# Kernel optimization log

Hardware: AMD Instinct MI355X
Metric: run time of the kernel (lower is better)

Reference implementation:

```python
import jax, jax.numpy as jnp
import numpy as np

HIDDEN = 4096
N_HEADS = 32
N_KV = 32
HEAD_DIM = HIDDEN // N_HEADS  # 128
T = 2048
THETA = 10000.0
EPS = 1e-5


def setup_inputs() -> dict:
    key = jax.random.key(0)
    ks = jax.random.split(key, 7)
    s = 0.02
    return {
        "positions": jnp.arange(T, dtype=jnp.int64),
        "hidden_states": jax.random.normal(ks[0], (T, HIDDEN), jnp.float32),
        "w_qkv": jax.random.normal(ks[1], ((N_HEADS + 2 * N_KV) * HEAD_DIM, HIDDEN), jnp.float32) * s,
        "w_o": jax.random.normal(ks[2], (HIDDEN, N_HEADS * HEAD_DIM), jnp.float32) * s,
        "q_norm_w": jnp.ones((N_HEADS, HEAD_DIM), jnp.float32) + jax.random.normal(ks[3], (N_HEADS, HEAD_DIM), jnp.float32) * s,
        "q_norm_b": jax.random.normal(ks[4], (N_HEADS, HEAD_DIM), jnp.float32) * s,
        "k_norm_w": jnp.ones((N_KV, HEAD_DIM), jnp.float32) + jax.random.normal(ks[5], (N_KV, HEAD_DIM), jnp.float32) * s,
        "k_norm_b": jax.random.normal(ks[6], (N_KV, HEAD_DIM), jnp.float32) * s,
    }


def _layer_norm_affine(x, w, b):
    # x: [T, H, d]; normalize over last dim, no affine inside, then per-head affine
    mu = jnp.mean(x, axis=-1, keepdims=True)
    var = jnp.var(x, axis=-1, keepdims=True)
    xn = (x - mu) * jax.lax.rsqrt(var + EPS)
    return xn * w + b


def _rope_neox(x, positions):
    # x: [T, H, d], NEOX style: rotate halves over full head_dim
    half = HEAD_DIM // 2
    inv_freq = 1.0 / (THETA ** (jnp.arange(0, half, dtype=jnp.float32) * 2.0 / HEAD_DIM))
    ang = positions.astype(jnp.float32)[:, None] * inv_freq  # [T, half]
    cos = jnp.cos(ang)[:, None, :]
    sin = jnp.sin(ang)[:, None, :]
    x1, x2 = x[..., :half], x[..., half:]
    return jnp.concatenate([x1 * cos - x2 * sin, x2 * cos + x1 * sin], axis=-1)


def reference(positions, hidden_states, w_qkv, w_o, q_norm_w, q_norm_b, k_norm_w, k_norm_b):
    qkv = hidden_states @ w_qkv.T  # [T, (H+2Hkv)*d]
    q_size = N_HEADS * HEAD_DIM
    kv_size = N_KV * HEAD_DIM
    q = qkv[:, :q_size].reshape(T, N_HEADS, HEAD_DIM)
    k = qkv[:, q_size:q_size + kv_size].reshape(T, N_KV, HEAD_DIM)
    v = qkv[:, q_size + kv_size:].reshape(T, N_KV, HEAD_DIM)

    q = _layer_norm_affine(q, q_norm_w, q_norm_b)
    k = _layer_norm_affine(k, k_norm_w, k_norm_b)
    q = _rope_neox(q, positions)
    k = _rope_neox(k, positions)

    scale = HEAD_DIM ** -0.5
    scores = jnp.einsum('thd,shd->hts', q, k) * scale  # [H, T, T]
    causal = jnp.tril(jnp.ones((T, T), dtype=bool))
    scores = jnp.where(causal[None], scores, jnp.finfo(scores.dtype).min)
    p = jax.nn.softmax(scores, axis=-1)
    attn = jnp.einsum('hts,shd->thd', p, v).reshape(T, N_HEADS * HEAD_DIM)
    return attn @ w_o.T
```

## Files before the change

### kernel.cpp

```cpp
#include <hip/hip_runtime.h>
#include <cstdint>

#define T_SEQ 2048
#define HID   4096
#define NH    32
#define HD    128
#define QKVW  12288

typedef float  f32x4  __attribute__((ext_vector_type(4)));
typedef __bf16 bf16x8 __attribute__((ext_vector_type(8)));

#define QSCALE (0.08838834764831845f * 1.4426950408889634f)

__device__ __forceinline__ unsigned short f2bf(float f) {
  unsigned int u = __builtin_bit_cast(unsigned int, f);
  u += 0x7fffu + ((u >> 16) & 1u);
  return (unsigned short)(u >> 16);
}
__device__ __forceinline__ float bf2f(unsigned short u) {
  return __builtin_bit_cast(float, (unsigned int)u << 16);
}

__device__ __forceinline__ void gload_lds16(const void* gptr, void* lptr) {
  __builtin_amdgcn_global_load_lds(
      (const __attribute__((address_space(1))) unsigned int*)(unsigned long long)(uintptr_t)gptr,
      (__attribute__((address_space(3))) unsigned int*)(unsigned int)(uintptr_t)lptr,
      16, 0, 0);
}

#define SB __builtin_amdgcn_sched_barrier(0)

__global__ __launch_bounds__(256) void cast_bf16(const float* __restrict__ in,
                                                 unsigned short* __restrict__ out,
                                                 int n4) {
  int i = blockIdx.x * 256 + threadIdx.x;
  int stride = gridDim.x * 256;
  for (; i < n4; i += stride) {
    float4 v = ((const float4*)in)[i];
    ushort4 o;
    o.x = f2bf(v.x); o.y = f2bf(v.y); o.z = f2bf(v.z); o.w = f2bf(v.w);
    ((ushort4*)out)[i] = o;
  }
}

__global__ __launch_bounds__(512, 2) void gemm_bt(const unsigned short* __restrict__ Ag,
                                                  const unsigned short* __restrict__ Bg,
                                                  float* __restrict__ C,
                                                  int M, int N, int K, int MT) {
  __shared__ unsigned short As_[2][128 * 64];
  __shared__ unsigned short Bs_[2][256 * 64];
  const int tid  = threadIdx.x;
  const int lane = tid & 63;
  const int w    = tid >> 6;
  const int wm   = w >> 2;
  const int wn   = w & 3;
  const int l15  = lane & 15;
  const int lg   = lane >> 4;

  const int nwg = gridDim.x;
  const int cpx = nwg >> 3;
  const int swz = (blockIdx.x & 7) * cpx + (blockIdx.x >> 3);
  const int bm  = (swz % MT) * 128;
  const int bn  = (swz / MT) * 256;
  const int nk  = K >> 6;

#define STAGE_A(buf, kt_) do {                                                   \
    const unsigned short* _s = Ag + (size_t)bm * K + (size_t)(kt_) * 64;         \
    _Pragma("unroll")                                                            \
    for (int _u = 0; _u < 2; ++_u) {                                             \
      const int _cid = _u * 512 + tid;                                           \
      const int _r = _cid >> 3, _ch = _cid & 7;                                  \
      gload_lds16(_s + (size_t)_r * K + ((_ch ^ (_r & 7)) * 8),                  \
                  &As_[buf][(_u * 512 + w * 64) * 8]);                           \
    } } while (0)

#define STAGE_B(buf, kt_) do {                                                   \
    const unsigned short* _s = Bg + (size_t)bn * K + (size_t)(kt_) * 64;         \
    _Pragma("unroll")                                                            \
    for (int _u = 0; _u < 4; ++_u) {                                             \
      const int _cid = _u * 512 + tid;                                           \
      const int _r = _cid >> 3, _ch = _cid & 7;                                  \
      gload_lds16(_s + (size_t)_r * K + ((_ch ^ (_r & 7)) * 8),                  \
                  &Bs_[buf][(_u * 512 + w * 64) * 8]);                           \
    } } while (0)

  f32x4 acc[4][4] = {};

  STAGE_A(0, 0);
  STAGE_B(0, 0);
  if (nk > 1) {
    STAGE_B(1, 1);
    asm volatile("s_waitcnt vmcnt(4)" ::: "memory");
  } else {
    asm volatile("s_waitcnt vmcnt(0)" ::: "memory");
  }
  __builtin_amdgcn_s_barrier();

  for (int t = 0; t < nk; ++t) {
    const int cur = t & 1;
    bf16x8 bfr[4][2];
#pragma unroll
    for (int n = 0; n < 4; ++n)
#pragma unroll
      for (int kk = 0; kk < 2; ++kk) {
        const int r = wn * 64 + n * 16 + l15;
        bfr[n][kk] = *(const bf16x8*)&Bs_[cur][r * 64 + (((kk * 4 + lg) ^ (r & 7)) * 8)];
      }
    bf16x8 a0[2][2];
#pragma unroll
    for (int mi = 0; mi < 2; ++mi)
#pragma unroll
      for (int kk = 0; kk < 2; ++kk) {
        const int r = wm * 64 + mi * 16 + l15;
        a0[mi][kk] = *(const bf16x8*)&As_[cur][r * 64 + (((kk * 4 + lg) ^ (r & 7)) * 8)];
      }
    if (t + 1 < nk) STAGE_A(cur ^ 1, t + 1);
    __builtin_amdgcn_s_barrier();
    __builtin_amdgcn_s_setprio(1);
#pragma unroll
    for (int mi = 0; mi < 2; ++mi)
#pragma unroll
      for (int n = 0; n < 4; ++n)
#pragma unroll
        for (int kk = 0; kk < 2; ++kk)
          acc[mi][n] = __builtin_amdgcn_mfma_f32_16x16x32_bf16(a0[mi][kk], bfr[n][kk], acc[mi][n], 0, 0, 0);
    __builtin_amdgcn_s_setprio(0);
    __builtin_amdgcn_s_barrier();

    bf16x8 a1[2][2];
#pragma unroll
    for (int mi = 0; mi < 2; ++mi)
#pragma unroll
      for (int kk = 0; kk < 2; ++kk) {
        const int r = wm * 64 + (2 + mi) * 16 + l15;
        a1[mi][kk] = *(const bf16x8*)&As_[cur][r * 64 + (((kk * 4 + lg) ^ (r & 7)) * 8)];
      }
    if (t + 2 < nk) STAGE_B(cur, t + 2);
    __builtin_amdgcn_s_barrier();
    __builtin_amdgcn_s_setprio(1);
#pragma unroll
    for (int mi = 0; mi < 2; ++mi)
#pragma unroll
      for (int n = 0; n < 4; ++n)
#pragma unroll
        for (int kk = 0; kk < 2; ++kk)
          acc[2 + mi][n] = __builtin_amdgcn_mfma_f32_16x16x32_bf16(a1[mi][kk], bfr[n][kk], acc[2 + mi][n], 0, 0, 0);
    __builtin_amdgcn_s_setprio(0);
    if (t + 1 < nk) {
      if (t + 2 < nk) asm volatile("s_waitcnt vmcnt(4)" ::: "memory");
      else            asm volatile("s_waitcnt vmcnt(0)" ::: "memory");
      __builtin_amdgcn_sched_barrier(0);
    }
    __builtin_amdgcn_s_barrier();
  }
#undef STAGE_A
#undef STAGE_B

#pragma unroll
  for (int m = 0; m < 4; ++m)
#pragma unroll
    for (int i = 0; i < 4; ++i) {
      const int row = bm + wm * 64 + m * 16 + lg * 4 + i;
#pragma unroll
      for (int n = 0; n < 4; ++n)
        C[(size_t)row * N + bn + wn * 64 + n * 16 + l15] = acc[m][n][i];
    }
}

__global__ __launch_bounds__(512, 2) void gemm_bt8(const unsigned short* __restrict__ Ag,
                                                   const unsigned short* __restrict__ Bg,
                                                   unsigned short* __restrict__ C,
                                                   int M, int N, int K, int MT) {
  __shared__ unsigned short As_[2][256 * 64];
  __shared__ unsigned short Bs_[2][192 * 64];
  const int tid  = threadIdx.x;
  const int lane = tid & 63;
  const int w    = tid >> 6;
  const int wm   = w & 3;
  const int wn   = w >> 2;
  const int l15  = lane & 15;
  const int lg   = lane >> 4;
  const int sw   = l15 & 7;

  const int cpx = gridDim.x >> 3;
  const int swz = (blockIdx.x & 7) * cpx + (blockIdx.x >> 3);
  const int bm  = (swz % MT) * 256;
  const int bn  = (swz / MT) * 192;
  const int nk  = K >> 6;

  const unsigned short* Abase = Ag + (size_t)bm * K;
  const unsigned short* Bbase = Bg + (size_t)bn * K;

#define SG(ldsbase, gbase, kt_, u_) do {                                        \
    const int _cid = (u_) * 512 + tid;                                          \
    const int _r = _cid >> 3, _ch = _cid & 7;                                   \
    gload_lds16((gbase) + (size_t)_r * K + (size_t)(kt_) * 64 +                 \
                    ((_ch ^ (_r & 7)) * 8),                                     \
                (void*)((char*)(ldsbase) + _cid * 16));                         \
  } while (0)
#define STAGE(abuf, bbuf, kt_) do {                                             \
    SG(abuf, Abase, kt_, 0); SG(abuf, Abase, kt_, 1);                           \
    SG(abuf, Abase, kt_, 2); SG(abuf, Abase, kt_, 3);                           \
    SG(bbuf, Bbase, kt_, 0); SG(bbuf, Bbase, kt_, 1);                           \
    SG(bbuf, Bbase, kt_, 2);                                                    \
  } while (0)

#define RD(base, r, kk)                                                          \
  (*(const bf16x8*)((const char*)(base) + (r) * 128 + ((((kk) * 4 + lg) ^ sw) * 16)))

#define MFMA24(afr, bfr) do {                                                    \
    _Pragma("unroll")                                                            \
    for (int _m = 0; _m < 4; ++_m)                                               \
      _Pragma("unroll")                                                          \
      for (int _n = 0; _n < 6; ++_n)                                             \
        acc[_m][_n] = __builtin_amdgcn_mfma_f32_16x16x32_bf16(                   \
            afr[_m], bfr[_n], acc[_m][_n], 0, 0, 0);                             \
  } while (0)

  f32x4 acc[4][6] = {};

  STAGE(As_[0], Bs_[0], 0);
  if (nk > 1) {
    STAGE(As_[1], Bs_[1], 1);
    asm volatile("s_waitcnt vmcnt(7)" ::: "memory");
  } else {
    asm volatile("s_waitcnt vmcnt(0)" ::: "memory");
  }
  SB;
  __builtin_amdgcn_s_barrier();

  for (int t = 0; t < nk; ++t) {
    const int cur = t & 1;
    const unsigned short* As = As_[cur];
    const unsigned short* Bs = Bs_[cur];
    bf16x8 a0[4], a1[4], b0[6], b1[6];

#pragma unroll
    for (int m = 0; m < 4; ++m) a0[m] = RD(As, wm * 64 + m * 16 + l15, 0);
#pragma unroll
    for (int n = 0; n < 6; ++n) b0[n] = RD(Bs, wn * 96 + n * 16 + l15, 0);
    SB;
#pragma unroll
    for (int m = 0; m < 4; ++m) a1[m] = RD(As, wm * 64 + m * 16 + l15, 1);
#pragma unroll
    for (int n = 0; n < 6; ++n) b1[n] = RD(Bs, wn * 96 + n * 16 + l15, 1);
    SB;
    asm volatile("s_waitcnt lgkmcnt(10)" ::: "memory");
    SB;
    __builtin_amdgcn_s_setprio(1);
    MFMA24(a0, b0);
    __builtin_amdgcn_s_setprio(0);
    SB;
    asm volatile("s_waitcnt lgkmcnt(0)" ::: "memory");
    SB;
    __builtin_amdgcn_s_barrier();
    if (t + 2 < nk) STAGE(As_[cur], Bs_[cur], t + 2);
    SB;
    __builtin_amdgcn_s_setprio(1);
    MFMA24(a1, b1);
    __builtin_amdgcn_s_setprio(0);
    if (t + 1 < nk) {
      if (t + 2 < nk) asm volatile("s_waitcnt vmcnt(7)" ::: "memory");
      else            asm volatile("s_waitcnt vmcnt(0)" ::: "memory");
      SB;
      __builtin_amdgcn_s_barrier();
    }
  }
#undef SG
#undef STAGE
#undef RD
#undef MFMA24

#pragma unroll
  for (int m = 0; m < 4; ++m)
#pragma unroll
    for (int i = 0; i < 4; ++i) {
      const int row = bm + wm * 64 + m * 16 + lg * 4 + i;
#pragma unroll
      for (int n = 0; n < 6; ++n)
        C[(size_t)row * N + bn + wn * 96 + n * 16 + l15] = f2bf(acc[m][n][i]);
    }
}

__global__ __launch_bounds__(256) void norm_rope(const unsigned short* __restrict__ qkv,
                                                 const float* __restrict__ qw,
                                                 const float* __restrict__ qb,
                                                 const float* __restrict__ kw,
                                                 const float* __restrict__ kb,
                                                 unsigned short* __restrict__ q,
                                                 unsigned short* __restrict__ k) {
  const int t    = blockIdx.x;
  const int tid  = threadIdx.x;
  const int lane = tid & 63;
  const int w    = tid >> 6;
  const float invf = exp2f(-(float)lane * (13.287712379549449f / 64.0f));
  const float ang  = (float)t * invf;
  const float c = cosf(ang), s = sinf(ang);
  const unsigned short* row = qkv + (size_t)t * QKVW;

#pragma unroll 1
  for (int sel = 0; sel < 2; ++sel) {
    const unsigned short* src = row + sel * HID;
    const float* wgt = sel ? kw : qw;
    const float* bia = sel ? kb : qb;
    unsigned short* dst = sel ? k : q;
    const float oscale = sel ? 1.0f : QSCALE;
    for (int h = w; h < NH; h += 4) {
      const unsigned short* x = src + h * HD;
      float x1 = bf2f(x[lane]), x2 = bf2f(x[lane + 64]);
      float sum = x1 + x2, ss = x1 * x1 + x2 * x2;
#pragma unroll
      for (int m = 1; m < 64; m <<= 1) {
        sum += __shfl_xor(sum, m, 64);
        ss  += __shfl_xor(ss, m, 64);
      }
      const float mu  = sum * (1.0f / 128.0f);
      const float var = ss * (1.0f / 128.0f) - mu * mu;
      const float r   = rsqrtf(var + 1e-5f);
      const float n1  = (x1 - mu) * r * wgt[h * HD + lane]      + bia[h * HD + lane];
      const float n2  = (x2 - mu) * r * wgt[h * HD + lane + 64] + bia[h * HD + lane + 64];
      const float o1  = (n1 * c - n2 * s) * oscale;
      const float o2  = (n2 * c + n1 * s) * oscale;
      dst[(size_t)t * HID + h * HD + lane]      = f2bf(o1);
      dst[(size_t)t * HID + h * HD + lane + 64] = f2bf(o2);
    }
  }
}

__global__ __launch_bounds__(256) void transpose_v(const unsigned short* __restrict__ v,
                                                   unsigned short* __restrict__ vt) {
  __shared__ unsigned short tile[64][65];
  const int h  = blockIdx.z;
  const int tt = blockIdx.x * 64;
  const int dd = blockIdx.y * 64;
  const int tid = threadIdx.x;
#pragma unroll
  for (int p = 0; p < 4; ++p) {
    int idx = p * 256 + tid;
    int r = idx >> 4, c4 = idx & 15;
    ushort4 val = *(const ushort4*)&v[(size_t)(tt + r) * QKVW + h * HD + dd + c4 * 4];
    tile[r][c4 * 4 + 0] = val.x;
    tile[r][c4 * 4 + 1] = val.y;
    tile[r][c4 * 4 + 2] = val.z;
    tile[r][c4 * 4 + 3] = val.w;
  }
  __syncthreads();
#pragma unroll
  for (int p = 0; p < 4; ++p) {
    int idx = p * 256 + tid;
    int r = idx >> 4, c4 = idx & 15;
    ushort4 o;
    o.x = tile[c4 * 4 + 0][r];
    o.y = tile[c4 * 4 + 1][r];
    o.z = tile[c4 * 4 + 2][r];
    o.w = tile[c4 * 4 + 3][r];
    *(ushort4*)&vt[((size_t)h * HD + dd + r) * T_SEQ + tt + c4 * 4] = o;
  }
}

__global__ __launch_bounds__(256) void attn_fwd(const unsigned short* __restrict__ Q,
                                                const unsigned short* __restrict__ K,
                                                const unsigned short* __restrict__ VT,
                                                unsigned short* __restrict__ O) {
  __shared__ unsigned short Ks[2][64 * 128];
  __shared__ unsigned short Vs[2][128 * 64];
  __shared__ unsigned short Ps[4][16 * 64];
  const int h    = blockIdx.y;
  const int pair = blockIdx.x;
  const int tid  = threadIdx.x;
  const int lane = tid & 63;
  const int w    = tid >> 6;
  const int l15  = lane & 15;
  const int lg   = lane >> 4;
  const int sw   = l15 & 7;

#pragma unroll 1
  for (int half = 0; half < 2; ++half) {
    const int qt   = half ? (31 - pair) : pair;
    const int qrow = qt * 64 + w * 16;

    bf16x8 qf[4];
#pragma unroll
    for (int kk = 0; kk < 4; ++kk)
      qf[kk] = *(const bf16x8*)&Q[(size_t)(qrow + l15) * HID + h * HD + kk * 32 + lg * 8];

    f32x4 o[8] = {};
    float mrow[4], lrow[4];
#pragma unroll
    for (int i = 0; i < 4; ++i) { mrow[i] = -1e30f; lrow[i] = 0.0f; }

    const int nkt = qt + 1;

    {
#pragma unroll
      for (int p = 0; p < 4; ++p) {
        const int c  = p * 256 + tid;
        const int kr = c >> 4, kc = c & 15;
        gload_lds16(&K[(size_t)kr * HID + h * HD + ((kc ^ (kr & 7)) * 8)],
                    &Ks[0][(p * 256 + w * 64) * 8]);
        const int vr = c >> 3, vc = c & 7;
        gload_lds16(&VT[((size_t)h * HD + vr) * T_SEQ + ((vc ^ (vr & 7)) * 8)],
                    &Vs[0][(p * 256 + w * 64) * 8]);
      }
    }
    __syncthreads();

#pragma unroll 1
    for (int kt = 0; kt < nkt; ++kt) {
      const int cur = kt & 1;
      if (kt + 1 < nkt) {
        const int k0 = (kt + 1) * 64;
#pragma unroll
        for (int p = 0; p < 4; ++p) {
          const int c  = p * 256 + tid;
          const int kr = c >> 4, kc = c & 15;
          gload_lds16(&K[(size_t)(k0 + kr) * HID + h * HD + ((kc ^ (kr & 7)) * 8)],
                      &Ks[cur ^ 1][(p * 256 + w * 64) * 8]);
          const int vr = c >> 3, vc = c & 7;
          gload_lds16(&VT[((size_t)h * HD + vr) * T_SEQ + k0 + ((vc ^ (vr & 7)) * 8)],
                      &Vs[cur ^ 1][(p * 256 + w * 64) * 8]);
        }
      }
      const unsigned short* ksb = Ks[cur];
      const unsigned short* vsb = Vs[cur];

      f32x4 sfr[4] = {};
#pragma unroll
      for (int n = 0; n < 4; ++n)
#pragma unroll
        for (int kk = 0; kk < 4; ++kk) {
          bf16x8 kf = *(const bf16x8*)&ksb[(n * 16 + l15) * 128 + ((kk * 4 + lg) ^ sw) * 8];
          sfr[n] = __builtin_amdgcn_mfma_f32_16x16x32_bf16(qf[kk], kf, sfr[n], 0, 0, 0);
        }

      if (kt == qt) {
#pragma unroll
        for (int n = 0; n < 4; ++n)
#pragma unroll
          for (int i = 0; i < 4; ++i)
            if (n * 16 + l15 > w * 16 + lg * 4 + i) sfr[n][i] = -1e30f;
      }

      float escale[4];
#pragma unroll
      for (int i = 0; i < 4; ++i) {
        float mx = fmaxf(fmaxf(sfr[0][i], sfr[1][i]), fmaxf(sfr[2][i], sfr[3][i]));
        mx = fmaxf(mx, __shfl_xor(mx, 1, 64));
        mx = fmaxf(mx, __shfl_xor(mx, 2, 64));
        mx = fmaxf(mx, __shfl_xor(mx, 4, 64));
        mx = fmaxf(mx, __shfl_xor(mx, 8, 64));
        const float mnew = fmaxf(mrow[i], mx);
        escale[i] = exp2f(mrow[i] - mnew);
        mrow[i] = mnew;
        const int prow = lg * 4 + i;
        float rs = 0.0f;
#pragma unroll
        for (int n = 0; n < 4; ++n) {
          const float p = exp2f(sfr[n][i] - mnew);
          rs += p;
          Ps[w][prow * 64 + (((2 * n + (l15 >> 3)) ^ (prow & 7)) * 8) + sw] = f2bf(p);
        }
        rs += __shfl_xor(rs, 1, 64);
        rs += __shfl_xor(rs, 2, 64);
        rs += __shfl_xor(rs, 4, 64);
        rs += __shfl_xor(rs, 8, 64);
        lrow[i] = lrow[i] * escale[i] + rs;
      }
#pragma unroll
      for (int f = 0; f < 8; ++f)
#pragma unroll
        for (int i = 0; i < 4; ++i) o[f][i] *= escale[i];

      asm volatile("s_waitcnt lgkmcnt(0)" ::: "memory");
      __builtin_amdgcn_sched_barrier(0);

      bf16x8 pf[2];
#pragma unroll
      for (int kk = 0; kk < 2; ++kk)
        pf[kk] = *(const bf16x8*)&Ps[w][l15 * 64 + ((kk * 4 + lg) ^ sw) * 8];
#pragma unroll
      for (int f = 0; f < 8; ++f)
#pragma unroll
        for (int kk = 0; kk < 2; ++kk) {
          bf16x8 vf = *(const bf16x8*)&vsb[(f * 16 + l15) * 64 + ((kk * 4 + lg) ^ sw) * 8];
          o[f] = __builtin_amdgcn_mfma_f32_16x16x32_bf16(pf[kk], vf, o[f], 0, 0, 0);
        }

      __syncthreads();
    }

#pragma unroll
    for (int i = 0; i < 4; ++i) {
      const float inv = 1.0f / lrow[i];
      const int trow = qrow + lg * 4 + i;
#pragma unroll
      for (int f = 0; f < 8; ++f)
        O[(size_t)trow * HID + h * HD + f * 16 + l15] = f2bf(o[f][i] * inv);
    }
  }
}

extern "C" void kernel_launch(void* const* d_in, const int* in_sizes, int n_in,
                              void* d_out, int out_size, void* d_ws, size_t ws_size,
                              hipStream_t stream) {
  const float* hidden = (const float*)d_in[1];
  const float* w_qkv  = (const float*)d_in[2];
  const float* w_o    = (const float*)d_in[3];
  const float* qw     = (const float*)d_in[4];
  const float* qb     = (const float*)d_in[5];
  const float* kw     = (const float*)d_in[6];
  const float* kb     = (const float*)d_in[7];

  char* ws = (char*)d_ws;
  unsigned short* wqkv_bf = (unsigned short*)(ws + 0);
  unsigned short* attn_bf = (unsigned short*)(ws + 0);
  unsigned short* wo_bf   = (unsigned short*)(ws + 16777216);
  unsigned short* hid_bf  = (unsigned short*)(ws + 100663296);
  unsigned short* vt_bf   = (unsigned short*)(ws + 100663296);
  unsigned short* qkv_bf  = (unsigned short*)(ws + 117440512);
  unsigned short* q_bf    = (unsigned short*)(ws + 167772160);
  unsigned short* k_bf    = (unsigned short*)(ws + 184549376);

  cast_bf16<<<2048, 256, 0, stream>>>(hidden, hid_bf, (T_SEQ * HID) / 4);
  cast_bf16<<<2048, 256, 0, stream>>>(w_qkv, wqkv_bf, (QKVW * HID) / 4);
  gemm_bt8<<<512, 512, 0, stream>>>(hid_bf, wqkv_bf, qkv_bf, T_SEQ, QKVW, HID, 8);
  cast_bf16<<<2048, 256, 0, stream>>>(w_o, wo_bf, (HID * HID) / 4);
  norm_rope<<<T_SEQ, 256, 0, stream>>>(qkv_bf, qw, qb, kw, kb, q_bf, k_bf);
  transpose_v<<<dim3(T_SEQ / 64, HD / 64, NH), 256, 0, stream>>>(qkv_bf + 2 * HID, vt_bf);
  attn_fwd<<<dim3(16, NH), 256, 0, stream>>>(q_bf, k_bf, vt_bf, attn_bf);
  gemm_bt<<<256, 512, 0, stream>>>(attn_bf, wo_bf, (float*)d_out, T_SEQ, HID, HID, 16);
}
```

Measured before the change: 463.8 us.

## Process two 16-row query fragments per warp in attention to reuse K/V tiles

Each warp now computes 32 query rows (two MFMA fragments) against each K/V tile, so a block covers 128 queries and the grid halves. This doubles MFMA work per LDS K/V fragment load and halves the global K/V traffic per query. In exchange it raises register pressure and halves the number of blocks, reducing occupancy and latency hiding.

After: 489.5 us. 5.6% more time.

```diff
diff --git a/kernel.cpp b/kernel.cpp
--- a/kernel.cpp
+++ b/kernel.cpp
@@ -364,9 +364,9 @@
                                                 unsigned short* __restrict__ O) {
   __shared__ unsigned short Ks[2][64 * 128];
   __shared__ unsigned short Vs[2][128 * 64];
-  __shared__ unsigned short Ps[4][16 * 64];
+  __shared__ unsigned short Ps[4][2][16 * 64];
   const int h    = blockIdx.y;
-  const int pair = blockIdx.x;
+  const int pr   = blockIdx.x;
   const int tid  = threadIdx.x;
   const int lane = tid & 63;
   const int w    = tid >> 6;
@@ -376,20 +376,24 @@
 
 #pragma unroll 1
   for (int half = 0; half < 2; ++half) {
-    const int qt   = half ? (31 - pair) : pair;
-    const int qrow = qt * 64 + w * 16;
-
-    bf16x8 qf[4];
-#pragma unroll
-    for (int kk = 0; kk < 4; ++kk)
-      qf[kk] = *(const bf16x8*)&Q[(size_t)(qrow + l15) * HID + h * HD + kk * 32 + lg * 8];
-
-    f32x4 o[8] = {};
-    float mrow[4], lrow[4];
-#pragma unroll
-    for (int i = 0; i < 4; ++i) { mrow[i] = -1e30f; lrow[i] = 0.0f; }
-
-    const int nkt = qt + 1;
+    const int jt    = half ? (15 - pr) : pr;
+    const int qbase = jt * 128 + w * 32;
+
+    bf16x8 qf[2][4];
+#pragma unroll
+    for (int f = 0; f < 2; ++f)
+#pragma unroll
+      for (int kk = 0; kk < 4; ++kk)
+        qf[f][kk] = *(const bf16x8*)&Q[(size_t)(qbase + f * 16 + l15) * HID + h * HD + kk * 32 + lg * 8];
+
+    f32x4 o[2][8] = {};
+    float mrow[2][4], lrow[2][4];
+#pragma unroll
+    for (int f = 0; f < 2; ++f)
+#pragma unroll
+      for (int i = 0; i < 4; ++i) { mrow[f][i] = -1e30f; lrow[f][i] = 0.0f; }
+
+    const int nkt = 2 * (jt + 1);
 
     {
 #pragma unroll
@@ -424,79 +428,91 @@
       const unsigned short* ksb = Ks[cur];
       const unsigned short* vsb = Vs[cur];
 
-      f32x4 sfr[4] = {};
+      f32x4 sfr[2][4] = {};
 #pragma unroll
       for (int n = 0; n < 4; ++n)
 #pragma unroll
         for (int kk = 0; kk < 4; ++kk) {
           bf16x8 kf = *(const bf16x8*)&ksb[(n * 16 + l15) * 128 + ((kk * 4 + lg) ^ sw) * 8];
-          sfr[n] = __builtin_amdgcn_mfma_f32_16x16x32_bf16(qf[kk], kf, sfr[n], 0, 0, 0);
+          sfr[0][n] = __builtin_amdgcn_mfma_f32_16x16x32_bf16(qf[0][kk], kf, sfr[0][n], 0, 0, 0);
+          sfr[1][n] = __builtin_amdgcn_mfma_f32_16x16x32_bf16(qf[1][kk], kf, sfr[1][n], 0, 0, 0);
         }
 
-      if (kt == qt) {
-#pragma unroll
-        for (int n = 0; n < 4; ++n)
-#pragma unroll
-          for (int i = 0; i < 4; ++i)
-            if (n * 16 + l15 > w * 16 + lg * 4 + i) sfr[n][i] = -1e30f;
-      }
-
-      float escale[4];
-#pragma unroll
-      for (int i = 0; i < 4; ++i) {
-        float mx = fmaxf(fmaxf(sfr[0][i], sfr[1][i]), fmaxf(sfr[2][i], sfr[3][i]));
-        mx = fmaxf(mx, __shfl_xor(mx, 1, 64));
-        mx = fmaxf(mx, __shfl_xor(mx, 2, 64));
-        mx = fmaxf(mx, __shfl_xor(mx, 4, 64));
-        mx = fmaxf(mx, __shfl_xor(mx, 8, 64));
-        const float mnew = fmaxf(mrow[i], mx);
-        escale[i] = exp2f(mrow[i] - mnew);
-        mrow[i] = mnew;
-        const int prow = lg * 4 + i;
-        float rs = 0.0f;
-#pragma unroll
-        for (int n = 0; n < 4; ++n) {
-          const float p = exp2f(sfr[n][i] - mnew);
-          rs += p;
-          Ps[w][prow * 64 + (((2 * n + (l15 >> 3)) ^ (prow & 7)) * 8) + sw] = f2bf(p);
+      if (kt >= 2 * jt) {
+#pragma unroll
+        for (int f = 0; f < 2; ++f)
+#pragma unroll
+          for (int n = 0; n < 4; ++n)
+#pragma unroll
+            for (int i = 0; i < 4; ++i)
+              if (kt * 64 + n * 16 + l15 > qbase + f * 16 + lg * 4 + i) sfr[f][n][i] = -1e30f;
+      }
+
+#pragma unroll
+      for (int f = 0; f < 2; ++f) {
+        float escale[4];
+#pragma unroll
+        for (int i = 0; i < 4; ++i) {
+          float mx = fmaxf(fmaxf(sfr[f][0][i], sfr[f][1][i]), fmaxf(sfr[f][2][i], sfr[f][3][i]));
+          mx = fmaxf(mx, __shfl_xor(mx, 1, 64));
+          mx = fmaxf(mx, __shfl_xor(mx, 2, 64));
+          mx = fmaxf(mx, __shfl_xor(mx, 4, 64));
+          mx = fmaxf(mx, __shfl_xor(mx, 8, 64));
+          const float mnew = fmaxf(mrow[f][i], mx);
+          escale[i] = exp2f(mrow[f][i] - mnew);
+          mrow[f][i] = mnew;
+          const int prow = lg * 4 + i;
+          float rs = 0.0f;
+#pragma unroll
+          for (int n = 0; n < 4; ++n) {
+            const float p = exp2f(sfr[f][n][i] - mnew);
+            rs += p;
+            Ps[w][f][prow * 64 + (((2 * n + (l15 >> 3)) ^ (prow & 7)) * 8) + sw] = f2bf(p);
+          }
+          rs += __shfl_xor(rs, 1, 64);
+          rs += __shfl_xor(rs, 2, 64);
+          rs += __shfl_xor(rs, 4, 64);
+          rs += __shfl_xor(rs, 8, 64);
+          lrow[f][i] = lrow[f][i] * escale[i] + rs;
         }
-        rs += __shfl_xor(rs, 1, 64);
-        rs += __shfl_xor(rs, 2, 64);
-        rs += __shfl_xor(rs, 4, 64);
-        rs += __shfl_xor(rs, 8, 64);
-        lrow[i] = lrow[i] * escale[i] + rs;
-      }
-#pragma unroll
-      for (int f = 0; f < 8; ++f)
-#pragma unroll
-        for (int i = 0; i < 4; ++i) o[f][i] *= escale[i];
+#pragma unroll
+        for (int fd = 0; fd < 8; ++fd)
+#pragma unroll
+          for (int i = 0; i < 4; ++i) o[f][fd][i] *= escale[i];
+      }
 
       asm volatile("s_waitcnt lgkmcnt(0)" ::: "memory");
       __builtin_amdgcn_sched_barrier(0);
 
-      bf16x8 pf[2];
-#pragma unroll
-      for (int kk = 0; kk < 2; ++kk)
-        pf[kk] = *(const bf16x8*)&Ps[w][l15 * 64 + ((kk * 4 + lg) ^ sw) * 8];
-#pragma unroll
-      for (int f = 0; f < 8; ++f)
+      bf16x8 pf[2][2];
+#pragma unroll
+      for (int f = 0; f < 2; ++f)
+#pragma unroll
+        for (int kk = 0; kk < 2; ++kk)
+          pf[f][kk] = *(const bf16x8*)&Ps[w][f][l15 * 64 + ((kk * 4 + lg) ^ sw) * 8];
+
+#pragma unroll
+      for (int fd = 0; fd < 8; ++fd)
 #pragma unroll
         for (int kk = 0; kk < 2; ++kk) {
-          bf16x8 vf = *(const bf16x8*)&vsb[(f * 16 + l15) * 64 + ((kk * 4 + lg) ^ sw) * 8];
-          o[f] = __builtin_amdgcn_mfma_f32_16x16x32_bf16(pf[kk], vf, o[f], 0, 0, 0);
+          bf16x8 vf = *(const bf16x8*)&vsb[(fd * 16 + l15) * 64 + ((kk * 4 + lg) ^ sw) * 8];
+          o[0][fd] = __builtin_amdgcn_mfma_f32_16x16x32_bf16(pf[0][kk], vf, o[0][fd], 0, 0, 0);
+          o[1][fd] = __builtin_amdgcn_mfma_f32_16x16x32_bf16(pf[1][kk], vf, o[1][fd], 0, 0, 0);
         }
 
       __syncthreads();
     }
 
 #pragma unroll
-    for (int i = 0; i < 4; ++i) {
-      const float inv = 1.0f / lrow[i];
-      const int trow = qrow + lg * 4 + i;
-#pragma unroll
-      for (int f = 0; f < 8; ++f)
-        O[(size_t)trow * HID + h * HD + f * 16 + l15] = f2bf(o[f][i] * inv);
-    }
+    for (int f = 0; f < 2; ++f)
+#pragma unroll
+      for (int i = 0; i < 4; ++i) {
+        const float inv = 1.0f / lrow[f][i];
+        const int trow = qbase + f * 16 + lg * 4 + i;
+#pragma unroll
+        for (int fd = 0; fd < 8; ++fd)
+          O[(size_t)trow * HID + h * HD + fd * 16 + l15] = f2bf(o[f][fd][i] * inv);
+      }
   }
 }
 
@@ -527,6 +543,6 @@
   cast_bf16<<<2048, 256, 0, stream>>>(w_o, wo_bf, (HID * HID) / 4);
   norm_rope<<<T_SEQ, 256, 0, stream>>>(qkv_bf, qw, qb, kw, kb, q_bf, k_bf);
   transpose_v<<<dim3(T_SEQ / 64, HD / 64, NH), 256, 0, stream>>>(qkv_bf + 2 * HID, vt_bf);
-  attn_fwd<<<dim3(16, NH), 256, 0, stream>>>(q_bf, k_bf, vt_bf, attn_bf);
+  attn_fwd<<<dim3(8, NH), 256, 0, stream>>>(q_bf, k_bf, vt_bf, attn_bf);
   gemm_bt<<<256, 512, 0, stream>>>(attn_bf, wo_bf, (float*)d_out, T_SEQ, HID, HID, 16);
 }
```

## Replace output-projection GEMM with 256x128-tile kernel using stage-ahead pipeline

Applied to the files above, without the earlier changes.

Swaps the output-projection GEMM from a 128x256 tile kernel to a 256x128 tile kernel modeled on the QKV GEMM. The new kernel loads the whole K-step of A and B fragments up front with explicit lgkmcnt waits and issues the next tile's global-to-LDS copy midway through the compute phase. The aim is fewer barriers per step and better overlap of loads with MFMA work. The tile shape change alters the grid mapping (MT=8), and it still uses 256 workgroups.

After: 459.0 us (median of 2 runs). About the same (-1.0%).

```diff
diff --git a/kernel.cpp b/kernel.cpp
--- a/kernel.cpp
+++ b/kernel.cpp
@@ -41,130 +41,6 @@
     o.x = f2bf(v.x); o.y = f2bf(v.y); o.z = f2bf(v.z); o.w = f2bf(v.w);
     ((ushort4*)out)[i] = o;
   }
-}
-
-__global__ __launch_bounds__(512, 2) void gemm_bt(const unsigned short* __restrict__ Ag,
-                                                  const unsigned short* __restrict__ Bg,
-                                                  float* __restrict__ C,
-                                                  int M, int N, int K, int MT) {
-  __shared__ unsigned short As_[2][128 * 64];
-  __shared__ unsigned short Bs_[2][256 * 64];
-  const int tid  = threadIdx.x;
-  const int lane = tid & 63;
-  const int w    = tid >> 6;
-  const int wm   = w >> 2;
-  const int wn   = w & 3;
-  const int l15  = lane & 15;
-  const int lg   = lane >> 4;
-
-  const int nwg = gridDim.x;
-  const int cpx = nwg >> 3;
-  const int swz = (blockIdx.x & 7) * cpx + (blockIdx.x >> 3);
-  const int bm  = (swz % MT) * 128;
-  const int bn  = (swz / MT) * 256;
-  const int nk  = K >> 6;
-
-#define STAGE_A(buf, kt_) do {                                                   \
-    const unsigned short* _s = Ag + (size_t)bm * K + (size_t)(kt_) * 64;         \
-    _Pragma("unroll")                                                            \
-    for (int _u = 0; _u < 2; ++_u) {                                             \
-      const int _cid = _u * 512 + tid;                                           \
-      const int _r = _cid >> 3, _ch = _cid & 7;                                  \
-      gload_lds16(_s + (size_t)_r * K + ((_ch ^ (_r & 7)) * 8),                  \
-                  &As_[buf][(_u * 512 + w * 64) * 8]);                           \
-    } } while (0)
-
-#define STAGE_B(buf, kt_) do {                                                   \
-    const unsigned short* _s = Bg + (size_t)bn * K + (size_t)(kt_) * 64;         \
-    _Pragma("unroll")                                                            \
-    for (int _u = 0; _u < 4; ++_u) {                                             \
-      const int _cid = _u * 512 + tid;                                           \
-      const int _r = _cid >> 3, _ch = _cid & 7;                                  \
-      gload_lds16(_s + (size_t)_r * K + ((_ch ^ (_r & 7)) * 8),                  \
-                  &Bs_[buf][(_u * 512 + w * 64) * 8]);                           \
-    } } while (0)
-
-  f32x4 acc[4][4] = {};
-
-  STAGE_A(0, 0);
-  STAGE_B(0, 0);
-  if (nk > 1) {
-    STAGE_B(1, 1);
-    asm volatile("s_waitcnt vmcnt(4)" ::: "memory");
-  } else {
-    asm volatile("s_waitcnt vmcnt(0)" ::: "memory");
-  }
-  __builtin_amdgcn_s_barrier();
-
-  for (int t = 0; t < nk; ++t) {
-    const int cur = t & 1;
-    bf16x8 bfr[4][2];
-#pragma unroll
-    for (int n = 0; n < 4; ++n)
-#pragma unroll
-      for (int kk = 0; kk < 2; ++kk) {
-        const int r = wn * 64 + n * 16 + l15;
-        bfr[n][kk] = *(const bf16x8*)&Bs_[cur][r * 64 + (((kk * 4 + lg) ^ (r & 7)) * 8)];
-      }
-    bf16x8 a0[2][2];
-#pragma unroll
-    for (int mi = 0; mi < 2; ++mi)
-#pragma unroll
-      for (int kk = 0; kk < 2; ++kk) {
-        const int r = wm * 64 + mi * 16 + l15;
-        a0[mi][kk] = *(const bf16x8*)&As_[cur][r * 64 + (((kk * 4 + lg) ^ (r & 7)) * 8)];
-      }
-    if (t + 1 < nk) STAGE_A(cur ^ 1, t + 1);
-    __builtin_amdgcn_s_barrier();
-    __builtin_amdgcn_s_setprio(1);
-#pragma unroll
-    for (int mi = 0; mi < 2; ++mi)
-#pragma unroll
-      for (int n = 0; n < 4; ++n)
-#pragma unroll
-        for (int kk = 0; kk < 2; ++kk)
-          acc[mi][n] = __builtin_amdgcn_mfma_f32_16x16x32_bf16(a0[mi][kk], bfr[n][kk], acc[mi][n], 0, 0, 0);
-    __builtin_amdgcn_s_setprio(0);
-    __builtin_amdgcn_s_barrier();
-
-    bf16x8 a1[2][2];
-#pragma unroll
-    for (int mi = 0; mi < 2; ++mi)
-#pragma unroll
-      for (int kk = 0; kk < 2; ++kk) {
-        const int r = wm * 64 + (2 + mi) * 16 + l15;
-        a1[mi][kk] = *(const bf16x8*)&As_[cur][r * 64 + (((kk * 4 + lg) ^ (r & 7)) * 8)];
-      }
-    if (t + 2 < nk) STAGE_B(cur, t + 2);
-    __builtin_amdgcn_s_barrier();
-    __builtin_amdgcn_s_setprio(1);
-#pragma unroll
-    for (int mi = 0; mi < 2; ++mi)
-#pragma unroll
-      for (int n = 0; n < 4; ++n)
-#pragma unroll
-        for (int kk = 0; kk < 2; ++kk)
-          acc[2 + mi][n] = __builtin_amdgcn_mfma_f32_16x16x32_bf16(a1[mi][kk], bfr[n][kk], acc[2 + mi][n], 0, 0, 0);
-    __builtin_amdgcn_s_setprio(0);
-    if (t + 1 < nk) {
-      if (t + 2 < nk) asm volatile("s_waitcnt vmcnt(4)" ::: "memory");
-      else            asm volatile("s_waitcnt vmcnt(0)" ::: "memory");
-      __builtin_amdgcn_sched_barrier(0);
-    }
-    __builtin_amdgcn_s_barrier();
-  }
-#undef STAGE_A
-#undef STAGE_B
-
-#pragma unroll
-  for (int m = 0; m < 4; ++m)
-#pragma unroll
-    for (int i = 0; i < 4; ++i) {
-      const int row = bm + wm * 64 + m * 16 + lg * 4 + i;
-#pragma unroll
-      for (int n = 0; n < 4; ++n)
-        C[(size_t)row * N + bn + wn * 64 + n * 16 + l15] = acc[m][n][i];
-    }
 }
 
 __global__ __launch_bounds__(512, 2) void gemm_bt8(const unsigned short* __restrict__ Ag,
@@ -279,6 +155,120 @@
 #pragma unroll
       for (int n = 0; n < 6; ++n)
         C[(size_t)row * N + bn + wn * 96 + n * 16 + l15] = f2bf(acc[m][n][i]);
+    }
+}
+
+__global__ __launch_bounds__(512, 2) void gemm2_bt8(const unsigned short* __restrict__ Ag,
+                                                    const unsigned short* __restrict__ Bg,
+                                                    float* __restrict__ C,
+                                                    int M, int N, int K, int MT) {
+  __shared__ unsigned short As_[2][256 * 64];
+  __shared__ unsigned short Bs_[2][128 * 64];
+  const int tid  = threadIdx.x;
+  const int lane = tid & 63;
+  const int w    = tid >> 6;
+  const int wm   = w & 3;
+  const int wn   = w >> 2;
+  const int l15  = lane & 15;
+  const int lg   = lane >> 4;
+  const int sw   = l15 & 7;
+
+  const int cpx = gridDim.x >> 3;
+  const int swz = (blockIdx.x & 7) * cpx + (blockIdx.x >> 3);
+  const int bm  = (swz % MT) * 256;
+  const int bn  = (swz / MT) * 128;
+  const int nk  = K >> 6;
+
+  const unsigned short* Abase = Ag + (size_t)bm * K;
+  const unsigned short* Bbase = Bg + (size_t)bn * K;
+
+#define SG(ldsbase, gbase, kt_, u_) do {                                        \
+    const int _cid = (u_) * 512 + tid;                                          \
+    const int _r = _cid >> 3, _ch = _cid & 7;                                   \
+    gload_lds16((gbase) + (size_t)_r * K + (size_t)(kt_) * 64 +                 \
+                    ((_ch ^ (_r & 7)) * 8),                                     \
+                (void*)((char*)(ldsbase) + _cid * 16));                         \
+  } while (0)
+#define STAGE(abuf, bbuf, kt_) do {                                             \
+    SG(abuf, Abase, kt_, 0); SG(abuf, Abase, kt_, 1);                           \
+    SG(abuf, Abase, kt_, 2); SG(abuf, Abase, kt_, 3);                           \
+    SG(bbuf, Bbase, kt_, 0); SG(bbuf, Bbase, kt_, 1);                           \
+  } while (0)
+
+#define RD(base, r, kk)                                                          \
+  (*(const bf16x8*)((const char*)(base) + (r) * 128 + ((((kk) * 4 + lg) ^ sw) * 16)))
+
+#define MFMA16(afr, bfr) do {                                                    \
+    _Pragma("unroll")                                                            \
+    for (int _m = 0; _m < 4; ++_m)                                               \
+      _Pragma("unroll")                                                          \
+      for (int _n = 0; _n < 4; ++_n)                                             \
+        acc[_m][_n] = __builtin_amdgcn_mfma_f32_16x16x32_bf16(                   \
+            afr[_m], bfr[_n], acc[_m][_n], 0, 0, 0);                             \
+  } while (0)
+
+  f32x4 acc[4][4] = {};
+
+  STAGE(As_[0], Bs_[0], 0);
+  if (nk > 1) {
+    STAGE(As_[1], Bs_[1], 1);
+    asm volatile("s_waitcnt vmcnt(6)" ::: "memory");
+  } else {
+    asm volatile("s_waitcnt vmcnt(0)" ::: "memory");
+  }
+  SB;
+  __builtin_amdgcn_s_barrier();
+
+  for (int t = 0; t < nk; ++t) {
+    const int cur = t & 1;
+    const unsigned short* As = As_[cur];
+    const unsigned short* Bs = Bs_[cur];
+    bf16x8 a0[4], a1[4], b0[4], b1[4];
+
+#pragma unroll
+    for (int m = 0; m < 4; ++m) a0[m] = RD(As, wm * 64 + m * 16 + l15, 0);
+#pragma unroll
+    for (int n = 0; n < 4; ++n) b0[n] = RD(Bs, wn * 64 + n * 16 + l15, 0);
+    SB;
+#pragma unroll
+    for (int m = 0; m < 4; ++m) a1[m] = RD(As, wm * 64 + m * 16 + l15, 1);
+#pragma unroll
+    for (int n = 0; n < 4; ++n) b1[n] = RD(Bs, wn * 64 + n * 16 + l15, 1);
+    SB;
+    asm volatile("s_waitcnt lgkmcnt(8)" ::: "memory");
+    SB;
+    __builtin_amdgcn_s_setprio(1);
+    MFMA16(a0, b0);
+    __builtin_amdgcn_s_setprio(0);
+    SB;
+    asm volatile("s_waitcnt lgkmcnt(0)" ::: "memory");
+    SB;
+    __builtin_amdgcn_s_barrier();
+    if (t + 2 < nk) STAGE(As_[cur], Bs_[cur], t + 2);
+    SB;
+    __builtin_amdgcn_s_setprio(1);
+    MFMA16(a1, b1);
+    __builtin_amdgcn_s_setprio(0);
+    if (t + 1 < nk) {
+      if (t + 2 < nk) asm volatile("s_waitcnt vmcnt(6)" ::: "memory");
+      else            asm volatile("s_waitcnt vmcnt(0)" ::: "memory");
+      SB;
+      __builtin_amdgcn_s_barrier();
+    }
+  }
+#undef SG
+#undef STAGE
+#undef RD
+#undef MFMA16
+
+#pragma unroll
+  for (int m = 0; m < 4; ++m)
+#pragma unroll
+    for (int i = 0; i < 4; ++i) {
+      const int row = bm + wm * 64 + m * 16 + lg * 4 + i;
+#pragma unroll
+      for (int n = 0; n < 4; ++n)
+        C[(size_t)row * N + bn + wn * 64 + n * 16 + l15] = acc[m][n][i];
     }
 }
 
@@ -528,5 +518,5 @@
   norm_rope<<<T_SEQ, 256, 0, stream>>>(qkv_bf, qw, qb, kw, kb, q_bf, k_bf);
   transpose_v<<<dim3(T_SEQ / 64, HD / 64, NH), 256, 0, stream>>>(qkv_bf + 2 * HID, vt_bf);
   attn_fwd<<<dim3(16, NH), 256, 0, stream>>>(q_bf, k_bf, vt_bf, attn_bf);
-  gemm_bt<<<256, 512, 0, stream>>>(attn_bf, wo_bf, (float*)d_out, T_SEQ, HID, HID, 16);
-}
+  gemm2_bt8<<<256, 512, 0, stream>>>(attn_bf, wo_bf, (float*)d_out, T_SEQ, HID, HID, 8);
+}
```
